# Optimization experiments

Hardware: AMD Instinct MI355X
Metric: run time of the kernel (lower is better)

## Reference

```python
import jax, jax.numpy as jnp
import numpy as np

C = 128                      # channels per irrep
LS = [0, 0, 1, 1, 2, 2]      # active irreps (0e,0o,1e,1o,2e,2o), sorted order
D = C * sum(2 * l + 1 for l in LS)  # 2304
N = 100000                   # nodes


def setup_inputs() -> dict:
    key = jax.random.key(0)
    ks = jax.random.split(key, 7)
    inp = {"x": jax.random.normal(ks[0], (N, D), dtype=jnp.float32)}
    scale = 1.0 / np.sqrt(C)
    for name, k in zip(["W0p", "W0m", "W1p", "W1m", "W2p", "W2m"], ks[1:]):
        inp[name] = jax.random.normal(k, (C, C), dtype=jnp.float32) * scale
    return inp


def reference(x, W0p, W0m, W1p, W1m, W2p, W2m):
    # Split flat features into per-(l,parity) blocks [N, C, 2l+1],
    # mix channels per irrep (movedim + Linear in torch == einsum here),
    # merge back and add residual.
    Ws = [W0p, W0m, W1p, W1m, W2p, W2m]
    idx = 0
    parts = []
    for l, W in zip(LS, Ws):
        d = C * (2 * l + 1)
        blk = x[:, idx:idx + d].reshape(-1, C, 2 * l + 1)  # [N, C, m]
        idx += d
        y = jnp.einsum('ncm,dc->ndm', blk, W)              # channel mix per m
        parts.append(y.reshape(-1, d))
    return x + jnp.concatenate(parts, axis=-1)
```

## Files before the change

### kernel.cpp

```cpp
#include <hip/hip_runtime.h>
#include <hip/hip_bf16.h>

typedef float f32x4 __attribute__((ext_vector_type(4)));
typedef short s16x8 __attribute__((ext_vector_type(8)));

__device__ __forceinline__ unsigned short f32_to_bf16(float f){
    union { float f; unsigned u; } v; v.f = f;
    unsigned r = v.u + 0x7fffu + ((v.u >> 16) & 1u);
    return (unsigned short)(r >> 16);
}
__device__ __forceinline__ unsigned pack2(float a, float b){
    float2 t; t.x = a; t.y = b;
    __hip_bfloat162 h = __float22bfloat162_rn(t);
    union { __hip_bfloat162 h; unsigned u; } c; c.h = h;
    return c.u;
}

template<int N> __device__ __forceinline__ void wait_vmcnt(){
    if constexpr (N == 0)       asm volatile("s_waitcnt vmcnt(0)"  ::: "memory");
    else if constexpr (N == 3)  asm volatile("s_waitcnt vmcnt(3)"  ::: "memory");
    else if constexpr (N == 4)  asm volatile("s_waitcnt vmcnt(4)"  ::: "memory");
    else if constexpr (N == 5)  asm volatile("s_waitcnt vmcnt(5)"  ::: "memory");
    else if constexpr (N == 8)  asm volatile("s_waitcnt vmcnt(8)"  ::: "memory");
    else static_assert(N == 0, "add wait case");
    __builtin_amdgcn_sched_barrier(0);
}

__device__ __forceinline__ void bar_sync(){
    asm volatile("s_waitcnt lgkmcnt(0)" ::: "memory");
    __builtin_amdgcn_s_barrier();
    __builtin_amdgcn_sched_barrier(0);
}

__device__ __forceinline__ void dma16(const float* g, float* l){
    __builtin_amdgcn_global_load_lds(
        (const __attribute__((address_space(1))) unsigned int*)g,
        (__attribute__((address_space(3))) unsigned int*)l, 16, 0, 0);
}

__global__ __launch_bounds__(256)
void wconv_kernel(const float* __restrict__ W0p, const float* __restrict__ W0m,
                  const float* __restrict__ W1p, const float* __restrict__ W1m,
                  const float* __restrict__ W2p, const float* __restrict__ W2m,
                  unsigned short* __restrict__ wbf)
{
    const int idx = blockIdx.x * 256 + threadIdx.x;
    const int w  = idx >> 14;
    const int rc = idx & 16383;
    const float* Wp;
    switch (w) {
        case 0: Wp = W0p; break;  case 1: Wp = W0m; break;
        case 2: Wp = W1p; break;  case 3: Wp = W1m; break;
        case 4: Wp = W2p; break;  default: Wp = W2m; break;
    }
    const float v = Wp[rc] + (((rc >> 7) == (rc & 127)) ? 1.0f : 0.0f);
    wbf[idx] = f32_to_bf16(v);
}

template<int ML, int NT>
__global__ __launch_bounds__(256, 3)
void lx_dma(const float* __restrict__ x, const unsigned short* __restrict__ wbf,
            float* __restrict__ out, int yoff0, int yoff1, int w0, int ntiles)
{
    constexpr int BLK   = 128 * ML;
    constexpr int NTB   = NT * BLK;
    constexpr int DI    = NTB * 4 / 4096;
    constexpr int SI    = DI;
    constexpr int RROWS = NT * ML;
    constexpr int RTC   = (RROWS + 15) / 16;
    constexpr int PR    = RTC * 16;
    constexpr int LDSS  = 136;
    constexpr int CPT   = NTB / 256;
    constexpr int V4    = CPT / 4;

    __shared__ __attribute__((aligned(16))) float          lin[NTB];
    __shared__ __attribute__((aligned(16))) unsigned short lbf[PR * LDSS];
    __shared__ __attribute__((aligned(16))) float          lout[NTB];

    const int parity = blockIdx.y;
    const int yoff   = parity ? yoff1 : yoff0;
    const unsigned short* wb = wbf + (size_t)(w0 + parity) * 16384;

    const int tid = threadIdx.x;
    const int wv  = tid >> 6, ln = tid & 63;
    const int l16 = ln & 15,  lhi = ln >> 4;

    s16x8 bfr[4][2];
    #pragma unroll
    for (int s = 0; s < 4; ++s)
        #pragma unroll
        for (int tf = 0; tf < 2; ++tf)
            bfr[s][tf] = *reinterpret_cast<const s16x8*>(
                wb + (wv * 32 + tf * 16 + l16) * 128 + s * 32 + lhi * 8);

    const int pnl = tid >> 5;
    const int pc0 = (tid & 31) * 4;

    auto dma_tile = [&](int t) {
        const float* gb = x + (size_t)t * NT * 2304 + yoff;
        #pragma unroll
        for (int j = 0; j < DI; ++j) {
            const int chunk = j * 4 + wv;
            const int dw = chunk * 256 + ln * 4;
            const int nl = dw / BLK;
            const int r  = dw - nl * BLK;
            dma16(gb + (size_t)nl * 2304 + r, &lin[chunk * 256]);
        }
    };
    auto flush_tile = [&](int t) {
        float* gb = out + (size_t)t * NT * 2304 + yoff;
        #pragma unroll
        for (int i = 0; i < SI; ++i) {
            const int dw = (i * 256 + tid) * 4;
            const int nl = dw / BLK;
            const int r  = dw - nl * BLK;
            *reinterpret_cast<float4*>(gb + (size_t)nl * 2304 + r) =
                *reinterpret_cast<const float4*>(&lout[dw]);
        }
    };

    int t = blockIdx.x;
    dma_tile(t);
    wait_vmcnt<0>();
    bar_sync();

    while (true) {
        {
            float v[CPT];
            const float* sp = &lin[pnl * BLK + pc0 * ML];
            #pragma unroll
            for (int i = 0; i < V4; ++i) {
                const float4 t4 = *reinterpret_cast<const float4*>(sp + i * 4);
                v[i*4+0] = t4.x; v[i*4+1] = t4.y; v[i*4+2] = t4.z; v[i*4+3] = t4.w;
            }
            #pragma unroll
            for (int mm = 0; mm < ML; ++mm) {
                unsigned* wp = reinterpret_cast<unsigned*>(&lbf[(pnl * ML + mm) * LDSS + pc0]);
                wp[0] = pack2(v[mm],          v[ML + mm]);
                wp[1] = pack2(v[2*ML + mm],   v[3*ML + mm]);
            }
        }
        bar_sync();

        const int nx = t + (int)gridDim.x;
        if (nx < ntiles) dma_tile(nx);

        f32x4 acc[RTC][2];
        #pragma unroll
        for (int rt = 0; rt < RTC; ++rt) {
            acc[rt][0] = (f32x4){0.f,0.f,0.f,0.f};
            acc[rt][1] = (f32x4){0.f,0.f,0.f,0.f};
        }
        #pragma unroll
        for (int s = 0; s < 4; ++s) {
            const int k0 = s * 32 + lhi * 8;
            #pragma unroll
            for (int rt = 0; rt < RTC; ++rt) {
                const s16x8 af = *reinterpret_cast<const s16x8*>(
                    &lbf[(rt * 16 + l16) * LDSS + k0]);
                acc[rt][0] = __builtin_amdgcn_mfma_f32_16x16x32_bf16(af, bfr[s][0], acc[rt][0], 0, 0, 0);
                acc[rt][1] = __builtin_amdgcn_mfma_f32_16x16x32_bf16(af, bfr[s][1], acc[rt][1], 0, 0, 0);
            }
        }

        #pragma unroll
        for (int rt = 0; rt < RTC; ++rt)
            #pragma unroll
            for (int tf = 0; tf < 2; ++tf) {
                const int col = wv * 32 + tf * 16 + l16;
                #pragma unroll
                for (int j = 0; j < 4; ++j) {
                    const int row = rt * 16 + lhi * 4 + j;
                    if (row < RROWS) {
                        const int nl = row / ML;
                        lout[nl * BLK + col * ML + (row - nl * ML)] = acc[rt][tf][j];
                    }
                }
            }
        bar_sync();

        flush_tile(t);

        if (nx >= ntiles) break;
        wait_vmcnt<SI>();
        bar_sync();
        t = nx;
    }
}

template<int WGS>
__global__ __launch_bounds__(256, 4)
void l0_dma(const float* __restrict__ x, const unsigned short* __restrict__ wbf,
            float* __restrict__ out, int ntiles)
{
    constexpr int NT = 16;
    constexpr int DI = 4;
    constexpr int SI = 4;

    __shared__ __attribute__((aligned(16))) float lin[2][NT * 256];

    const int tid = threadIdx.x;
    const int wv  = tid >> 6, ln = tid & 63;
    const int l16 = ln & 15,  lhi = ln >> 4;
    const int b     = wv >> 1;
    const int dbase = (wv & 1) * 64;
    const unsigned short* wb = wbf + b * 16384;

    s16x8 afr[4][4];
    #pragma unroll
    for (int s = 0; s < 4; ++s)
        #pragma unroll
        for (int dt = 0; dt < 4; ++dt)
            afr[s][dt] = *reinterpret_cast<const s16x8*>(
                wb + (dbase + dt * 16 + l16) * 128 + s * 32 + lhi * 8);

    auto dma_tile = [&](int t, int cur) {
        const float* gb = x + (size_t)t * NT * 2304;
        float* lb = &lin[cur][0];
        #pragma unroll
        for (int j = 0; j < DI; ++j) {
            const int chunk = j * 4 + wv;
            const int dw   = chunk * 256 + ln * 4;
            const int node = dw >> 8;
            const int r    = dw & 255;
            dma16(gb + (size_t)node * 2304 + (r ^ ((node & 7) << 2)), lb + chunk * 256);
        }
    };

    const int tstart = blockIdx.x;
    int cur = 0;
    dma_tile(tstart, 0);
    if (tstart + WGS < ntiles) { dma_tile(tstart + WGS, 1); wait_vmcnt<DI>(); }
    else                       { wait_vmcnt<0>(); }
    bar_sync();

    for (int t = tstart; t < ntiles; t += WGS, cur ^= 1) {
        const bool has1 = (t + WGS)     < ntiles;
        const bool has2 = (t + 2 * WGS) < ntiles;

        f32x4 acc[4];
        #pragma unroll
        for (int dt = 0; dt < 4; ++dt) acc[dt] = (f32x4){0.f,0.f,0.f,0.f};

        const float* bp = &lin[cur][0];
        const int nb = l16 * 256;
        const int sw = (l16 & 7) << 2;
        #pragma unroll
        for (int s = 0; s < 4; ++s) {
            const int c0 = b * 128 + s * 32 + lhi * 8;
            const float4 v0 = *reinterpret_cast<const float4*>(&bp[nb + ((c0    ) ^ sw)]);
            const float4 v1 = *reinterpret_cast<const float4*>(&bp[nb + ((c0 + 4) ^ sw)]);
            union { s16x8 v; unsigned u[4]; } bf;
            bf.u[0] = pack2(v0.x, v0.y); bf.u[1] = pack2(v0.z, v0.w);
            bf.u[2] = pack2(v1.x, v1.y); bf.u[3] = pack2(v1.z, v1.w);
            #pragma unroll
            for (int dt = 0; dt < 4; ++dt)
                acc[dt] = __builtin_amdgcn_mfma_f32_16x16x32_bf16(afr[s][dt], bf.v, acc[dt], 0, 0, 0);
        }

        bar_sync();

        float* dst = out + ((size_t)t * NT + l16) * 2304 + b * 128 + dbase + lhi * 4;
        #pragma unroll
        for (int dt = 0; dt < 4; ++dt) {
            float4 vv; vv.x = acc[dt][0]; vv.y = acc[dt][1];
                       vv.z = acc[dt][2]; vv.w = acc[dt][3];
            *reinterpret_cast<float4*>(dst + dt * 16) = vv;
        }

        if (has2) dma_tile(t + 2 * WGS, cur);
        if (has1) { if (has2) wait_vmcnt<SI + DI>(); else wait_vmcnt<SI>(); }
        bar_sync();
    }
}

extern "C" void kernel_launch(void* const* d_in, const int* in_sizes, int n_in,
                              void* d_out, int out_size, void* d_ws, size_t ws_size,
                              hipStream_t stream) {
    const float* x   = (const float*)d_in[0];
    const float* W0p = (const float*)d_in[1];
    const float* W0m = (const float*)d_in[2];
    const float* W1p = (const float*)d_in[3];
    const float* W1m = (const float*)d_in[4];
    const float* W2p = (const float*)d_in[5];
    const float* W2m = (const float*)d_in[6];
    float* out = (float*)d_out;
    unsigned short* wbf = (unsigned short*)d_ws;

    const int N = in_sizes[0] / 2304;

    wconv_kernel<<<384, 256, 0, stream>>>(W0p, W0m, W1p, W1m, W2p, W2m, wbf);

    lx_dma<5, 8><<<dim3(384, 2), 256, 0, stream>>>(x, wbf, out, 1024, 1664, 4, N / 8);
    lx_dma<3, 8><<<dim3(384, 2), 256, 0, stream>>>(x, wbf, out, 256,  640,  2, N / 8);
    l0_dma<1024><<<1024,         256, 0, stream>>>(x, wbf, out, N / 16);
}
```

Baseline: 399.6 us.

## Double-buffer input tiles in lx_dma to prefetch two tiles ahead

Result: faster. 389.9 us, median of 2 (-2.4%).

```diff
diff --git a/kernel.cpp b/kernel.cpp
--- a/kernel.cpp
+++ b/kernel.cpp
@@ -22,6 +22,8 @@
     else if constexpr (N == 4)  asm volatile("s_waitcnt vmcnt(4)"  ::: "memory");
     else if constexpr (N == 5)  asm volatile("s_waitcnt vmcnt(5)"  ::: "memory");
     else if constexpr (N == 8)  asm volatile("s_waitcnt vmcnt(8)"  ::: "memory");
+    else if constexpr (N == 9)  asm volatile("s_waitcnt vmcnt(9)"  ::: "memory");
+    else if constexpr (N == 15) asm volatile("s_waitcnt vmcnt(15)" ::: "memory");
     else static_assert(N == 0, "add wait case");
     __builtin_amdgcn_sched_barrier(0);
 }
@@ -57,8 +59,8 @@
     wbf[idx] = f32_to_bf16(v);
 }
 
-template<int ML, int NT>
-__global__ __launch_bounds__(256, 3)
+template<int ML, int NT, int OCC>
+__global__ __launch_bounds__(256, OCC)
 void lx_dma(const float* __restrict__ x, const unsigned short* __restrict__ wbf,
             float* __restrict__ out, int yoff0, int yoff1, int w0, int ntiles)
 {
@@ -73,7 +75,7 @@
     constexpr int CPT   = NTB / 256;
     constexpr int V4    = CPT / 4;
 
-    __shared__ __attribute__((aligned(16))) float          lin[NTB];
+    __shared__ __attribute__((aligned(16))) float          lin[2][NTB];
     __shared__ __attribute__((aligned(16))) unsigned short lbf[PR * LDSS];
     __shared__ __attribute__((aligned(16))) float          lout[NTB];
 
@@ -96,7 +98,7 @@
     const int pnl = tid >> 5;
     const int pc0 = (tid & 31) * 4;
 
-    auto dma_tile = [&](int t) {
+    auto dma_tile = [&](int t, int cur) {
         const float* gb = x + (size_t)t * NT * 2304 + yoff;
         #pragma unroll
         for (int j = 0; j < DI; ++j) {
@@ -104,7 +106,7 @@
             const int dw = chunk * 256 + ln * 4;
             const int nl = dw / BLK;
             const int r  = dw - nl * BLK;
-            dma16(gb + (size_t)nl * 2304 + r, &lin[chunk * 256]);
+            dma16(gb + (size_t)nl * 2304 + r, &lin[cur][chunk * 256]);
         }
     };
     auto flush_tile = [&](int t) {
@@ -119,15 +121,17 @@
         }
     };
 
-    int t = blockIdx.x;
-    dma_tile(t);
-    wait_vmcnt<0>();
+    const int G = (int)gridDim.x;
+    int t = blockIdx.x, cur = 0;
+    dma_tile(t, 0);
+    if (t + G < ntiles) { dma_tile(t + G, 1); wait_vmcnt<DI>(); }
+    else                { wait_vmcnt<0>(); }
     bar_sync();
 
     while (true) {
         {
             float v[CPT];
-            const float* sp = &lin[pnl * BLK + pc0 * ML];
+            const float* sp = &lin[cur][pnl * BLK + pc0 * ML];
             #pragma unroll
             for (int i = 0; i < V4; ++i) {
                 const float4 t4 = *reinterpret_cast<const float4*>(sp + i * 4);
@@ -142,8 +146,7 @@
         }
         bar_sync();
 
-        const int nx = t + (int)gridDim.x;
-        if (nx < ntiles) dma_tile(nx);
+        if (t + 2 * G < ntiles) dma_tile(t + 2 * G, cur);
 
         f32x4 acc[RTC][2];
         #pragma unroll
@@ -181,10 +184,10 @@
 
         flush_tile(t);
 
-        if (nx >= ntiles) break;
-        wait_vmcnt<SI>();
-        bar_sync();
-        t = nx;
+        if (t + G >= ntiles) break;
+        wait_vmcnt<2 * SI + DI>();
+        bar_sync();
+        t += G; cur ^= 1;
     }
 }
 
@@ -230,7 +233,7 @@
     const int tstart = blockIdx.x;
     int cur = 0;
     dma_tile(tstart, 0);
-    if (tstart + WGS < ntiles) { dma_tile(tstart + WGS, 1); wait_vmcnt<DI>(); }
+    if (tstart + WGS < ntiles) { dma_tile(tstart + WGS, 1); wait_vmcnt<4>(); }
     else                       { wait_vmcnt<0>(); }
     bar_sync();
 
@@ -269,7 +272,7 @@
         }
 
         if (has2) dma_tile(t + 2 * WGS, cur);
-        if (has1) { if (has2) wait_vmcnt<SI + DI>(); else wait_vmcnt<SI>(); }
+        if (has1) { if (has2) wait_vmcnt<8>(); else wait_vmcnt<4>(); }
         bar_sync();
     }
 }
@@ -291,7 +294,7 @@
 
     wconv_kernel<<<384, 256, 0, stream>>>(W0p, W0m, W1p, W1m, W2p, W2m, wbf);
 
-    lx_dma<5, 8><<<dim3(384, 2), 256, 0, stream>>>(x, wbf, out, 1024, 1664, 4, N / 8);
-    lx_dma<3, 8><<<dim3(384, 2), 256, 0, stream>>>(x, wbf, out, 256,  640,  2, N / 8);
-    l0_dma<1024><<<1024,         256, 0, stream>>>(x, wbf, out, N / 16);
-}
+    lx_dma<5, 8, 2><<<dim3(256, 2), 256, 0, stream>>>(x, wbf, out, 1024, 1664, 4, N / 8);
+    lx_dma<3, 8, 3><<<dim3(384, 2), 256, 0, stream>>>(x, wbf, out, 256,  640,  2, N / 8);
+    l0_dma<1024>   <<<1024,         256, 0, stream>>>(x, wbf, out, N / 16);
+}
```
